# Kernel optimization log

Hardware: AMD Instinct MI355X
Metric: run time of the kernel (lower is better)

Reference implementation:

```python
import jax, jax.numpy as jnp
import numpy as np

S, B, IN, OUT = 2048, 8, 1024, 4096
ALPHA = 0.5  # SmoothQuant migration strength (scaling_factor)
QMAX = 127.0  # symmetric int8


def _ste_round(t):
    # straight-through round (matches pytorch_quantization fake-quant)
    return t + jax.lax.stop_gradient(jnp.round(t) - t)


def _fake_quant(t):
    # per-tensor symmetric int8 fake quantization
    amax = jax.lax.stop_gradient(jnp.max(jnp.abs(t)))
    s = jnp.where(amax > 0, amax / QMAX, jnp.float32(1.0))
    return jnp.clip(_ste_round(t / s), -QMAX, QMAX) * s


def setup_inputs() -> dict:
    key = jax.random.key(0)
    k1, k2, k3 = jax.random.split(key, 3)
    x = jax.random.normal(k1, (S, B, IN), dtype=jnp.float32)
    weight = jax.random.normal(k2, (OUT, IN), dtype=jnp.float32) * 0.02
    bias = jax.random.normal(k3, (OUT,), dtype=jnp.float32) * 0.01
    return {"x": x, "weight": weight, "bias": bias}


def reference(x, weight, bias):
    seq, bs, _ = x.shape
    x2 = x.reshape(-1, IN)  # [S*B, IN]
    # dynamic per-input-channel scales (detached in the original)
    w_scale = jnp.max(jnp.abs(jax.lax.stop_gradient(weight)), axis=0)   # [IN]
    act_scale = jnp.max(jnp.abs(jax.lax.stop_gradient(x2)), axis=0)     # [IN]
    scale = act_scale ** ALPHA / w_scale ** (1.0 - ALPHA)
    scale = jnp.where(scale == 0, jnp.float32(1.0), scale)
    w = _fake_quant(weight * scale)   # [OUT, IN]
    xq = _fake_quant(x2 / scale)      # [S*B, IN]
    out = xq @ w.T + bias[None, :]    # [S*B, OUT]
    return out.reshape(-1, bs, OUT)
```

## Files before the change

kernel.cpp:

```cpp
#include <hip/hip_runtime.h>

#define IN_DIM  1024
#define OUT_DIM 4096
#define M_DIM   16384
#define QMAXF   127.0f

typedef int v4i __attribute__((ext_vector_type(4)));

__global__ void colmax4_kernel(const float4* __restrict__ in, unsigned* __restrict__ outb,
                               int rows, int rpb) {
    int t  = threadIdx.x;
    int r0 = blockIdx.x * rpb;
    int r1 = r0 + rpb; if (r1 > rows) r1 = rows;
    float m0 = 0.f, m1 = 0.f, m2 = 0.f, m3 = 0.f;
    #pragma unroll 4
    for (int r = r0; r < r1; ++r) {
        float4 v = in[(size_t)r * 256 + t];
        m0 = fmaxf(m0, fabsf(v.x));
        m1 = fmaxf(m1, fabsf(v.y));
        m2 = fmaxf(m2, fabsf(v.z));
        m3 = fmaxf(m3, fabsf(v.w));
    }
    unsigned* o = outb + t * 4;
    atomicMax(o + 0, __float_as_uint(m0));
    atomicMax(o + 1, __float_as_uint(m1));
    atomicMax(o + 2, __float_as_uint(m2));
    atomicMax(o + 3, __float_as_uint(m3));
}

__global__ void scale_amax_kernel(float* __restrict__ wsf) {
    int j = threadIdx.x;
    float wsc = wsf[j];
    float asc = wsf[1024 + j];
    float s = sqrtf(asc) / sqrtf(wsc);
    if (s == 0.0f) s = 1.0f;
    wsf[2048 + j] = s;
    float aw = wsc * s;
    float ax = asc / s;
    int lane = j & 63, wid = j >> 6;
    #pragma unroll
    for (int off = 32; off; off >>= 1) {
        aw = fmaxf(aw, __shfl_down(aw, off));
        ax = fmaxf(ax, __shfl_down(ax, off));
    }
    __shared__ float rw[16], rx[16];
    if (lane == 0) { rw[wid] = aw; rx[wid] = ax; }
    __syncthreads();
    if (j == 0) {
        float mw = rw[0], mx = rx[0];
        #pragma unroll
        for (int i = 1; i < 16; ++i) { mw = fmaxf(mw, rw[i]); mx = fmaxf(mx, rx[i]); }
        wsf[3072] = mw;
        wsf[3073] = mx;
    }
}

#define NW4 (OUT_DIM * IN_DIM / 4)
#define NX4 (M_DIM * IN_DIM / 4)

__device__ __forceinline__ unsigned pack_q4(float t0, float t1, float t2, float t3, float qs) {
    int q0 = (int)fminf(fmaxf(rintf(t0 / qs), -QMAXF), QMAXF);
    int q1 = (int)fminf(fmaxf(rintf(t1 / qs), -QMAXF), QMAXF);
    int q2 = (int)fminf(fmaxf(rintf(t2 / qs), -QMAXF), QMAXF);
    int q3 = (int)fminf(fmaxf(rintf(t3 / qs), -QMAXF), QMAXF);
    return (q0 & 0xff) | ((q1 & 0xff) << 8) | ((q2 & 0xff) << 16) | ((q3 & 0xff) << 24);
}

__global__ void quant_fused_kernel(const float4* __restrict__ w, const float4* __restrict__ x,
                                   const float* __restrict__ wsf,
                                   unsigned* __restrict__ w8, unsigned* __restrict__ x8) {
    const float4* scale4 = (const float4*)(wsf + 2048);
    float amw = wsf[3072], amx = wsf[3073];
    float qsw = amw > 0.f ? amw / QMAXF : 1.0f;
    float qsx = amx > 0.f ? amx / QMAXF : 1.0f;
    int stride = gridDim.x * blockDim.x;
    for (int i = blockIdx.x * blockDim.x + threadIdx.x; i < NW4 + NX4; i += stride) {
        if (i < NW4) {
            float4 v = w[i];
            float4 s = scale4[i & 255];
            w8[i] = pack_q4(v.x * s.x, v.y * s.y, v.z * s.z, v.w * s.w, qsw);
        } else {
            int k = i - NW4;
            float4 v = x[k];
            float4 s = scale4[k & 255];
            x8[k] = pack_q4(v.x / s.x, v.y / s.y, v.z / s.z, v.w / s.w, qsx);
        }
    }
}

#define BM 128
#define BN 128
#define BK 128

__device__ __forceinline__ void load_lds16(const void* g, void* l) {
    __builtin_amdgcn_global_load_lds((const __attribute__((address_space(1))) void*)g,
                                     (__attribute__((address_space(3))) void*)l, 16, 0, 0);
}

__global__ __launch_bounds__(256) void gemm_i8_kernel(
    const char* __restrict__ Xq, const char* __restrict__ Wq,
    const float* __restrict__ bias, const float* __restrict__ wsf,
    float* __restrict__ out) {
    __shared__ char As[BM * BK];
    __shared__ char Bs[BN * BK];
    const int K = IN_DIM, N = OUT_DIM;
    int tid  = threadIdx.x;
    int lane = tid & 63, w = tid >> 6;

    int lin = blockIdx.y * gridDim.x + blockIdx.x;
    int swz = (lin & 7) * 512 + (lin >> 3);
    int bn0 = (swz & 31) * BN, bm0 = (swz >> 5) * BM;

    int wrow = (w >> 1) * 64, wcol = (w & 1) * 64;
    int l15 = lane & 15, l4 = lane >> 4;
    int swzl = (lane & 7) << 4;

    v4i acc[4][4];
    #pragma unroll
    for (int i = 0; i < 4; ++i)
        #pragma unroll
        for (int jj = 0; jj < 4; ++jj)
            acc[i][jj] = (v4i){0, 0, 0, 0};

    for (int kt = 0; kt < K / BK; ++kt) {
        int k0 = kt * BK;
        #pragma unroll
        for (int q = 0; q < 4; ++q) {
            int c = q * 256 + w * 64 + lane;
            int row = c >> 3, slot = c & 7;
            int col = (slot * 16) ^ ((row & 7) << 4);
            load_lds16(Xq + (size_t)(bm0 + row) * K + k0 + col, As + q * 4096 + w * 1024);
            load_lds16(Wq + (size_t)(bn0 + row) * K + k0 + col, Bs + q * 4096 + w * 1024);
        }
        __syncthreads();
        #pragma unroll
        for (int kk = 0; kk < 2; ++kk) {
            int coff = ((kk << 6) | (l4 << 4)) ^ swzl;
            v4i a[4], b[4];
            #pragma unroll
            for (int am = 0; am < 4; ++am)
                a[am] = *(const v4i*)(As + (wrow + am * 16 + l15) * BK + coff);
            #pragma unroll
            for (int bb = 0; bb < 4; ++bb)
                b[bb] = *(const v4i*)(Bs + (wcol + bb * 16 + l15) * BK + coff);
            #pragma unroll
            for (int am = 0; am < 4; ++am)
                #pragma unroll
                for (int bb = 0; bb < 4; ++bb)
                    acc[am][bb] = __builtin_amdgcn_mfma_i32_16x16x64_i8(a[am], b[bb], acc[am][bb], 0, 0, 0);
        }
        __syncthreads();
    }

    float amw = wsf[3072], amx = wsf[3073];
    float sw = amw > 0.f ? amw / QMAXF : 1.0f;
    float sx = amx > 0.f ? amx / QMAXF : 1.0f;
    float sp = sw * sx;

    #pragma unroll
    for (int am = 0; am < 4; ++am) {
        int row = bm0 + wrow + am * 16 + l4 * 4;
        #pragma unroll
        for (int bb = 0; bb < 4; ++bb) {
            int col = bn0 + wcol + bb * 16 + l15;
            float bv = bias[col];
            #pragma unroll
            for (int r = 0; r < 4; ++r)
                out[(size_t)(row + r) * N + col] = fmaf(sp, (float)acc[am][bb][r], bv);
        }
    }
}

extern "C" void kernel_launch(void* const* d_in, const int* in_sizes, int n_in,
                              void* d_out, int out_size, void* d_ws, size_t ws_size,
                              hipStream_t stream) {
    const float* x      = (const float*)d_in[0];
    const float* weight = (const float*)d_in[1];
    const float* bias   = (const float*)d_in[2];
    float* out = (float*)d_out;

    float*    wsf = (float*)d_ws;
    unsigned* wsu = (unsigned*)d_ws;
    char* X8 = (char*)d_ws + 16384;
    char* W8 = X8 + (size_t)M_DIM * IN_DIM;

    hipMemsetAsync(d_ws, 0, 16384, stream);

    colmax4_kernel<<<256, 256, 0, stream>>>((const float4*)weight, wsu,        OUT_DIM, 16);
    colmax4_kernel<<<256, 256, 0, stream>>>((const float4*)x,      wsu + 1024, M_DIM,   64);

    scale_amax_kernel<<<1, 1024, 0, stream>>>(wsf);

    quant_fused_kernel<<<2560, 256, 0, stream>>>((const float4*)weight, (const float4*)x,
                                                 wsf, (unsigned*)W8, (unsigned*)X8);

    gemm_i8_kernel<<<dim3(OUT_DIM / BN, M_DIM / BM), 256, 0, stream>>>(X8, W8, bias, wsf, out);
}
```

Before: 462.1 us.

## Rewrite int8 GEMM as 256x256 tile with 4-stage LDS pipeline

Replaces the 128x128x128 int8 GEMM with a 256x256x64 tile run by 512 threads. It uses a 4-buffer LDS ring with two tiles prefetched via global_load_lds, split A/B loads interleaved with MFMA phases, explicit vmcnt waits and s_setprio around compute. The aim is to overlap global loads with MFMA work and to raise arithmetic intensity per block. In exchange it carries high register pressure (128 accumulator VGPRs per thread) and 128KB of LDS per block, which may limit occupancy despite launch_bounds(512,2).

```diff
diff --git a/kernel.cpp b/kernel.cpp
--- a/kernel.cpp
+++ b/kernel.cpp
@@ -88,68 +88,117 @@
     }
 }
 
-#define BM 128
-#define BN 128
-#define BK 128
+#define GBM 256
+#define GBN 256
+#define GBK 64
+#define GNT (IN_DIM / GBK)
 
 __device__ __forceinline__ void load_lds16(const void* g, void* l) {
     __builtin_amdgcn_global_load_lds((const __attribute__((address_space(1))) void*)g,
                                      (__attribute__((address_space(3))) void*)l, 16, 0, 0);
 }
 
-__global__ __launch_bounds__(256) void gemm_i8_kernel(
+#define MFMA_I8 __builtin_amdgcn_mfma_i32_16x16x64_i8
+#define FENCE() asm volatile("" ::: "memory")
+
+__global__ __launch_bounds__(512, 2) void gemm_i8_256(
     const char* __restrict__ Xq, const char* __restrict__ Wq,
     const float* __restrict__ bias, const float* __restrict__ wsf,
     float* __restrict__ out) {
-    __shared__ char As[BM * BK];
-    __shared__ char Bs[BN * BK];
+    __shared__ char sA[4][GBM * GBK];
+    __shared__ char sB[4][GBN * GBK];
     const int K = IN_DIM, N = OUT_DIM;
     int tid  = threadIdx.x;
     int lane = tid & 63, w = tid >> 6;
+    int l15  = lane & 15, l4 = lane >> 4;
 
     int lin = blockIdx.y * gridDim.x + blockIdx.x;
-    int swz = (lin & 7) * 512 + (lin >> 3);
-    int bn0 = (swz & 31) * BN, bm0 = (swz >> 5) * BM;
-
-    int wrow = (w >> 1) * 64, wcol = (w & 1) * 64;
-    int l15 = lane & 15, l4 = lane >> 4;
-    int swzl = (lane & 7) << 4;
-
-    v4i acc[4][4];
-    #pragma unroll
-    for (int i = 0; i < 4; ++i)
-        #pragma unroll
-        for (int jj = 0; jj < 4; ++jj)
-            acc[i][jj] = (v4i){0, 0, 0, 0};
-
-    for (int kt = 0; kt < K / BK; ++kt) {
-        int k0 = kt * BK;
-        #pragma unroll
-        for (int q = 0; q < 4; ++q) {
-            int c = q * 256 + w * 64 + lane;
-            int row = c >> 3, slot = c & 7;
-            int col = (slot * 16) ^ ((row & 7) << 4);
-            load_lds16(Xq + (size_t)(bm0 + row) * K + k0 + col, As + q * 4096 + w * 1024);
-            load_lds16(Wq + (size_t)(bn0 + row) * K + k0 + col, Bs + q * 4096 + w * 1024);
-        }
-        __syncthreads();
-        #pragma unroll
-        for (int kk = 0; kk < 2; ++kk) {
-            int coff = ((kk << 6) | (l4 << 4)) ^ swzl;
-            v4i a[4], b[4];
+    int swz = (lin & 7) * 128 + (lin >> 3);
+    int bn0 = (swz & 15) * GBN;
+    int bm0 = (swz >> 4) * GBM;
+
+    int wm = w >> 2, wn = w & 3;
+
+    size_t srcA[2], srcB[2];
+    int dstOff[2];
+    #pragma unroll
+    for (int i = 0; i < 2; ++i) {
+        int chunk = w * 128 + i * 64 + lane;
+        int row = chunk >> 2, slot = chunk & 3;
+        int col = (slot * 16) ^ ((row & 3) << 4);
+        srcA[i]   = (size_t)(bm0 + row) * K + col;
+        srcB[i]   = (size_t)(bn0 + row) * K + col;
+        dstOff[i] = (w * 128 + i * 64) * 16;
+    }
+
+    int xorv  = ((l4 ^ (l15 & 3)) << 4);
+    int aBase = (wm * 128 + l15) * 64 + xorv;
+    int bBase = (wn * 64  + l15) * 64 + xorv;
+
+    v4i acc[8][4];
+    #pragma unroll
+    for (int i = 0; i < 8; ++i)
+        #pragma unroll
+        for (int j = 0; j < 4; ++j)
+            acc[i][j] = (v4i){0, 0, 0, 0};
+
+    #pragma unroll
+    for (int tt = 0; tt < 2; ++tt) {
+        #pragma unroll
+        for (int i = 0; i < 2; ++i) load_lds16(Xq + srcA[i] + tt * GBK, sA[tt] + dstOff[i]);
+        #pragma unroll
+        for (int i = 0; i < 2; ++i) load_lds16(Wq + srcB[i] + tt * GBK, sB[tt] + dstOff[i]);
+    }
+    asm volatile("s_waitcnt vmcnt(4)");
+    __builtin_amdgcn_s_barrier();
+    FENCE();
+
+    for (int t = 0; t < GNT; ++t) {
+        const int rb = t & 3, sb = (t + 2) & 3;
+        const char* A = sA[rb];
+        const char* B = sB[rb];
+        const bool st = (t + 2 < GNT);
+        v4i a[4], b[4];
+
+        #pragma unroll
+        for (int i = 0; i < 4; ++i) a[i] = *(const v4i*)(A + aBase + (i * 16) * 64);
+        #pragma unroll
+        for (int i = 0; i < 4; ++i) b[i] = *(const v4i*)(B + bBase + i * 1024);
+        if (st) {
+            load_lds16(Xq + srcA[0] + (t + 2) * GBK, sA[sb] + dstOff[0]);
+            load_lds16(Xq + srcA[1] + (t + 2) * GBK, sA[sb] + dstOff[1]);
+        }
+        __builtin_amdgcn_s_barrier();
+        FENCE();
+        __builtin_amdgcn_s_setprio(1);
+        #pragma unroll
+        for (int am = 0; am < 4; ++am)
             #pragma unroll
-            for (int am = 0; am < 4; ++am)
-                a[am] = *(const v4i*)(As + (wrow + am * 16 + l15) * BK + coff);
+            for (int bn = 0; bn < 4; ++bn)
+                acc[am][bn] = MFMA_I8(a[am], b[bn], acc[am][bn], 0, 0, 0);
+        __builtin_amdgcn_s_setprio(0);
+        __builtin_amdgcn_s_barrier();
+        FENCE();
+
+        #pragma unroll
+        for (int i = 0; i < 4; ++i) a[i] = *(const v4i*)(A + aBase + (64 + i * 16) * 64);
+        if (st) {
+            load_lds16(Wq + srcB[0] + (t + 2) * GBK, sB[sb] + dstOff[0]);
+            load_lds16(Wq + srcB[1] + (t + 2) * GBK, sB[sb] + dstOff[1]);
+        }
+        __builtin_amdgcn_s_barrier();
+        FENCE();
+        __builtin_amdgcn_s_setprio(1);
+        #pragma unroll
+        for (int am = 0; am < 4; ++am)
             #pragma unroll
-            for (int bb = 0; bb < 4; ++bb)
-                b[bb] = *(const v4i*)(Bs + (wcol + bb * 16 + l15) * BK + coff);
-            #pragma unroll
-            for (int am = 0; am < 4; ++am)
-                #pragma unroll
-                for (int bb = 0; bb < 4; ++bb)
-                    acc[am][bb] = __builtin_amdgcn_mfma_i32_16x16x64_i8(a[am], b[bb], acc[am][bb], 0, 0, 0);
-        }
-        __syncthreads();
+            for (int bn = 0; bn < 4; ++bn)
+                acc[4 + am][bn] = MFMA_I8(a[am], b[bn], acc[4 + am][bn], 0, 0, 0);
+        __builtin_amdgcn_s_setprio(0);
+        if (t < GNT - 2)       asm volatile("s_waitcnt vmcnt(4)");
+        else if (t == GNT - 2) asm volatile("s_waitcnt vmcnt(0)");
+        __builtin_amdgcn_s_barrier();
+        FENCE();
     }
 
     float amw = wsf[3072], amx = wsf[3073];
@@ -158,15 +207,15 @@
     float sp = sw * sx;
 
     #pragma unroll
-    for (int am = 0; am < 4; ++am) {
-        int row = bm0 + wrow + am * 16 + l4 * 4;
-        #pragma unroll
-        for (int bb = 0; bb < 4; ++bb) {
-            int col = bn0 + wcol + bb * 16 + l15;
+    for (int am = 0; am < 8; ++am) {
+        int row = bm0 + wm * 128 + am * 16 + l4 * 4;
+        #pragma unroll
+        for (int bn = 0; bn < 4; ++bn) {
+            int col = bn0 + wn * 64 + bn * 16 + l15;
             float bv = bias[col];
             #pragma unroll
             for (int r = 0; r < 4; ++r)
-                out[(size_t)(row + r) * N + col] = fmaf(sp, (float)acc[am][bb][r], bv);
+                out[(size_t)(row + r) * N + col] = fmaf(sp, (float)acc[am][bn][r], bv);
         }
     }
 }
@@ -194,5 +243,5 @@
     quant_fused_kernel<<<2560, 256, 0, stream>>>((const float4*)weight, (const float4*)x,
                                                  wsf, (unsigned*)W8, (unsigned*)X8);
 
-    gemm_i8_kernel<<<dim3(OUT_DIM / BN, M_DIM / BM), 256, 0, stream>>>(X8, W8, bias, wsf, out);
-}
+    gemm_i8_256<<<dim3(OUT_DIM / GBN, M_DIM / GBM), 512, 0, stream>>>(X8, W8, bias, wsf, out);
+}
```

After: 462.4 us. About the same (+0.1%).
